# Kernel optimization log

Hardware: AMD Instinct MI355X
Metric: run time of the kernel (lower is better)

## Reference

```python
import jax, jax.numpy as jnp
import numpy as np

SHIFT, REDUCE = 3, 2
B, L, E, H = 64, 512, 300, 256


def _make_transitions():
    # Left-branching valid parse: S S R S R S R ... (L shifts, L-1 reduces)
    T = 2 * L - 1
    tr = np.full(T, REDUCE, dtype=np.int64)
    tr[0] = SHIFT
    tr[1::2] = SHIFT
    return jnp.asarray(np.tile(tr[None, :], (B, 1)))


def setup_inputs() -> dict:
    key = jax.random.key(0)
    ks = jax.random.split(key, 5)
    s = 0.05
    return {
        "sentence": jax.random.normal(ks[0], (B, L, E), jnp.float32),
        "transitions": _make_transitions(),
        "W_word": jax.random.normal(ks[1], (E, 2 * H), jnp.float32) * s,
        "b_word": jnp.zeros((2 * H,), jnp.float32),
        "W_left": jax.random.normal(ks[2], (H, 5 * H), jnp.float32) * s,
        "W_right": jax.random.normal(ks[3], (H, 5 * H), jnp.float32) * s,
        "b_reduce": jnp.zeros((5 * H,), jnp.float32),
    }


def reference(sentence, transitions, W_word, b_word, W_left, W_right, b_reduce):
    Bsz, Ls, _ = sentence.shape
    Hs = W_left.shape[0]
    proj = sentence @ W_word + b_word                  # [B, L, 2H] (word projection; BN/dropout disabled)
    h_buf, c_buf = jnp.split(proj, 2, axis=2)          # buffers, each [B, L, H]
    T = transitions.shape[1]
    bidx = jnp.arange(Bsz)

    def step(carry, trans_t):
        sh, sc, ptr, bp = carry                        # thin stacks [B,T+2,H], pointers [B]
        shift = trans_t == SHIFT
        i1 = jnp.maximum(ptr - 1, 0)                   # right child (stack top)
        i2 = jnp.maximum(ptr - 2, 0)                   # left child
        hl, cl = sh[bidx, i2], sc[bidx, i2]
        hr, cr = sh[bidx, i1], sc[bidx, i1]
        g = hl @ W_left + hr @ W_right + b_reduce      # [B, 5H] TreeLSTM gates
        ig, flg, frg, og, ug = jnp.split(g, 5, axis=1)
        c_red = (jax.nn.sigmoid(flg) * cl + jax.nn.sigmoid(frg) * cr
                 + jax.nn.sigmoid(ig) * jnp.tanh(ug))
        h_red = jax.nn.sigmoid(og) * jnp.tanh(c_red)
        bsafe = jnp.minimum(bp, Ls - 1)
        val_h = jnp.where(shift[:, None], h_buf[bidx, bsafe], h_red)
        val_c = jnp.where(shift[:, None], c_buf[bidx, bsafe], c_red)
        pos = jnp.where(shift, ptr, i2)                # shift pushes at ptr; reduce writes at ptr-2
        sh = sh.at[bidx, pos].set(val_h)
        sc = sc.at[bidx, pos].set(val_c)
        ptr = ptr + jnp.where(shift, 1, -1)
        bp = bp + shift.astype(bp.dtype)
        return (sh, sc, ptr, bp), None

    sh0 = jnp.zeros((Bsz, T + 2, Hs), sentence.dtype)
    sc0 = jnp.zeros((Bsz, T + 2, Hs), sentence.dtype)
    ptr0 = jnp.zeros((Bsz,), jnp.int32)
    bp0 = jnp.zeros((Bsz,), jnp.int32)
    (sh, sc, ptr, _), _ = jax.lax.scan(
        step, (sh0, sc0, ptr0, bp0), jnp.swapaxes(transitions, 0, 1))
    return sh[bidx, jnp.maximum(ptr - 1, 0)]           # final stack top h: [B, H]
```

## Files before the change

### kernel.cpp

```cpp
#include <hip/hip_runtime.h>
#include <hip/hip_bf16.h>
#include <math.h>

#define BSZ   64
#define LSEQ  512
#define EDIM  300
#define HDIM  256
#define TLEN  1023
#define PROJW 512
#define GW    1280

#define NROW  8
#define NHID  8
#define RGBLK 32
#define NRG   8
#define NBLK  256
#define SLOTS 2

#define PROJ_N   (BSZ*LSEQ*PROJW)
#define STACKF   PROJ_N
#define STACK_N  (2*BSZ*SLOTS*2*HDIM)
#define FLAG_OFF (STACKF + STACK_N)
#define FLAGS_N  1024
#define ARR_OFF  (FLAG_OFF + FLAGS_N)
#define ARR_STRIDE 16

#define NODEBIT 0x80000000u
#define SENT    0xFFFFFFFFu
#define LROW    264
#define WPITCH  641

__global__ void __launch_bounds__(256)
proj_gemm(const float* __restrict__ A, const float* __restrict__ W,
          const float* __restrict__ bias, float* __restrict__ out) {
    __shared__ float As[8][65];
    __shared__ float Bs[8][64];
    const int tid = threadIdx.x;
    const int tx = tid & 15, ty = tid >> 4;
    const int bm = blockIdx.y, bn = blockIdx.x;

    float acc[4][4] = {};
    const int e  = tid * 2;
    const int ar = e >> 3, ac = e & 7;
    const int br = e >> 6, bc = e & 63;

    for (int k0 = 0; k0 < EDIM; k0 += 8) {
        __syncthreads();
        {
            const float* Ap = A + (size_t)(bm * 64 + ar) * EDIM;
            int gk = k0 + ac;
            As[ac][ar]     = (gk     < EDIM) ? Ap[gk]     : 0.f;
            As[ac + 1][ar] = (gk + 1 < EDIM) ? Ap[gk + 1] : 0.f;
            int gkb = k0 + br;
            float w0 = 0.f, w1 = 0.f;
            if (gkb < EDIM) {
                const float* Wp = W + (size_t)gkb * PROJW + bn * 64;
                w0 = Wp[bc]; w1 = Wp[bc + 1];
            }
            Bs[br][bc] = w0; Bs[br][bc + 1] = w1;
        }
        __syncthreads();
        #pragma unroll
        for (int kk = 0; kk < 8; ++kk) {
            float a[4], b[4];
            #pragma unroll
            for (int i = 0; i < 4; ++i) a[i] = As[kk][ty * 4 + i];
            #pragma unroll
            for (int j = 0; j < 4; ++j) b[j] = Bs[kk][tx * 4 + j];
            #pragma unroll
            for (int i = 0; i < 4; ++i)
                #pragma unroll
                for (int j = 0; j < 4; ++j)
                    acc[i][j] += a[i] * b[j];
        }
    }
    #pragma unroll
    for (int i = 0; i < 4; ++i) {
        const int row  = bm * 64 + ty * 4 + i;
        const int col0 = bn * 64 + tx * 4;
        float* op = out + (size_t)row * PROJW + col0;
        #pragma unroll
        for (int j = 0; j < 4; ++j) op[j] = acc[i][j] + bias[col0 + j];
    }
}

__global__ void flags_kernel(const int* __restrict__ trans, int* __restrict__ flags) {
    const int t = blockIdx.x * 256 + threadIdx.x;
    if (t >= TLEN) return;
    int f = 0;
    for (int b = 0; b < BSZ; ++b) f |= (trans[(size_t)b * TLEN + t] != 3) ? 1 : 0;
    flags[t] = f;
}

__device__ __forceinline__ unsigned encodeH(short tag, int slot, int grow) {
    if (tag >= 0)  return (unsigned)(((size_t)grow * LSEQ + (int)tag) * PROJW);
    if (tag <= -3) return SENT;
    const int par = (tag == -2) ? 1 : 0;
    return NODEBIT | (unsigned)(STACKF + ((par * BSZ + grow) * SLOTS + slot) * (2 * HDIM));
}

__device__ __forceinline__ float cohLoad(const float* ws, unsigned off) {
    return __uint_as_float(__hip_atomic_load((const unsigned*)ws + off,
                          __ATOMIC_RELAXED, __HIP_MEMORY_SCOPE_AGENT));
}
__device__ __forceinline__ float2 cohLoad2(const float* ws, unsigned off) {
    unsigned long long v = __hip_atomic_load((const unsigned long long*)(ws + off),
                          __ATOMIC_RELAXED, __HIP_MEMORY_SCOPE_AGENT);
    union { unsigned long long u; float2 f; } cv; cv.u = v;
    return cv.f;
}
__device__ __forceinline__ void cohStore(float* ws, unsigned off, float v) {
    __hip_atomic_store((unsigned*)ws + off, __float_as_uint(v),
                       __ATOMIC_RELAXED, __HIP_MEMORY_SCOPE_AGENT);
}

__device__ __forceinline__ float loadC(const float* ws, unsigned oh, int gn) {
    if (oh == SENT) return 0.f;
    if (oh & NODEBIT) return cohLoad(ws, (oh & ~NODEBIT) + HDIM + gn);
    return ws[oh + HDIM + gn];
}

__device__ __forceinline__ void stage_rows(float* __restrict__ buf,
    const unsigned* __restrict__ desc, const int* __restrict__ isred,
    const float* __restrict__ ws, int srow, int sc, bool nodePhase) {
    if (!isred[srow]) return;
    const unsigned oh = desc[srow];
    const int m = srow & 7;
    if (!nodePhase) {
        if (oh == SENT) {
            const float4 z = make_float4(0.f, 0.f, 0.f, 0.f);
            #pragma unroll
            for (int j = 0; j < 2; ++j) {
                const int Q = sc + 32 * j;
                *(float4*)&buf[srow * LROW + 4 * (Q ^ m)] = z;
            }
        } else if (!(oh & NODEBIT)) {
            const float4* s = (const float4*)(ws + oh);
            #pragma unroll
            for (int j = 0; j < 2; ++j) {
                const int Q = sc + 32 * j;
                *(float4*)&buf[srow * LROW + 4 * (Q ^ m)] = s[Q];
            }
        }
    } else if (oh != SENT && (oh & NODEBIT)) {
        const unsigned base = oh & ~NODEBIT;
        #pragma unroll
        for (int j = 0; j < 2; ++j) {
            const int Q = sc + 32 * j;
            const float2 lo = cohLoad2(ws, base + 4 * Q);
            const float2 hi = cohLoad2(ws, base + 4 * Q + 2);
            *(float4*)&buf[srow * LROW + 4 * (Q ^ m)] = make_float4(lo.x, lo.y, hi.x, hi.y);
        }
    }
}

__global__ void __launch_bounds__(256, 1)
scan_coop(const int* __restrict__ trans,
          const float* __restrict__ Wl, const float* __restrict__ Wr,
          const float* __restrict__ bred,
          float* __restrict__ ws, float* __restrict__ out) {
    __shared__ float4 wpack[NHID * WPITCH];
    __shared__ __align__(16) float hls[NROW * LROW];
    __shared__ __align__(16) float hrs[NROW * LROW];
    __shared__ __align__(16) float red[8 * NROW * NHID * 5];
    __shared__ unsigned tbits[NROW][32];
    __shared__ unsigned fbits[32];
    __shared__ short    tg[NROW][SLOTS];
    __shared__ unsigned d_hl[NROW], d_hr[NROW], d_wr[NROW], d_oh[NROW];
    __shared__ int      isred[NROW];

    const int tid   = threadIdx.x;
    const int cs    = blockIdx.x & 31;
    const int rg    = blockIdx.x >> 5;
    const int rbase = rg * NROW;
    const int n0    = cs * NHID;

    const int srow = tid >> 5, sc = tid & 31;
    const int colq = tid & 7;
    const int t4   = (tid >> 3) & 3;
    const int w8   = tid >> 5;

    const int* flags  = (const int*)(ws + FLAG_OFF);
    unsigned*  arr    = (unsigned*)(ws + ARR_OFF);
    unsigned*  myslot = &arr[(size_t)blockIdx.x * ARR_STRIDE];

    for (int idx = tid; idx < NHID * 640; idx += 256) {
        const int g = idx % 10, kq = (idx / 10) & 63, c = idx / 640;
        const int col  = n0 + c;
        const int gate = (g < 5) ? g : g - 5;
        const float* src = (g < 5) ? Wl : Wr;
        const int k0 = kq * 4;
        float4 v;
        v.x = src[(size_t)(k0 + 0) * GW + gate * HDIM + col];
        v.y = src[(size_t)(k0 + 1) * GW + gate * HDIM + col];
        v.z = src[(size_t)(k0 + 2) * GW + gate * HDIM + col];
        v.w = src[(size_t)(k0 + 3) * GW + gate * HDIM + col];
        wpack[c * WPITCH + kq * 10 + g] = v;
    }
    if (tid < NROW * 32) {
        const int r2 = tid >> 5, w = tid & 31;
        unsigned bits = 0;
        for (int j = 0; j < 32; ++j) {
            const int t = w * 32 + j;
            if (t < TLEN && trans[(size_t)(rbase + r2) * TLEN + t] == 3) bits |= (1u << j);
        }
        tbits[r2][w] = bits;
    }
    if (tid < 32) {
        unsigned bits = 0;
        for (int j = 0; j < 32; ++j) {
            const int t = tid * 32 + j;
            if (t < TLEN && flags[t]) bits |= (1u << j);
        }
        fbits[tid] = bits;
    }
    if (tid < NROW) {
        tg[tid][0] = -3; tg[tid][1] = -3;
        isred[tid] = 0;
    }

    float bv[5];
    #pragma unroll
    for (int g = 0; g < 5; ++g) bv[g] = bred[g * HDIM + n0 + colq];

    int ptr = 0, bp = 0;
    unsigned nbar = 0;
    __syncthreads();

    for (int t = 0; t < TLEN; ++t) {
        if (tid < NROW) {
            const int r = tid, grow = rbase + r;
            const int is_shift = (tbits[r][t >> 5] >> (t & 31)) & 1;
            if (is_shift) {
                int pos = ptr; if (pos < 0) pos = 0; if (pos > SLOTS - 1) pos = SLOTS - 1;
                tg[r][pos] = (short)min(bp, LSEQ - 1);
                ptr++; bp++;
                isred[r] = 0;
            } else {
                const int i1 = min(max(ptr - 1, 0), SLOTS - 1);
                const int i2 = min(max(ptr - 2, 0), SLOTS - 1);
                const short t1 = tg[r][i1], t2 = tg[r][i2];
                d_hl[r] = encodeH(t2, i2, grow);
                d_hr[r] = encodeH(t1, i1, grow);
                const int pnew = (t2 == -1) ? 1 : 0;
                d_wr[r] = (unsigned)(STACKF + ((pnew * BSZ + grow) * SLOTS + i2) * (2 * HDIM));
                tg[r][i2] = (short)(pnew ? -2 : -1);
                ptr--;
                isred[r] = 1;
            }
        }
        __syncthreads();

        if (!((fbits[t >> 5] >> (t & 31)) & 1)) continue;
        ++nbar;

        stage_rows(hls, d_hl, isred, ws, srow, sc, false);
        stage_rows(hrs, d_hr, isred, ws, srow, sc, false);

        if (tid < RGBLK) {
            const unsigned* slot = &arr[(size_t)(rg * RGBLK + tid) * ARR_STRIDE];
            while (__hip_atomic_load(slot, __ATOMIC_RELAXED, __HIP_MEMORY_SCOPE_AGENT) < nbar - 1)
                __builtin_amdgcn_s_sleep(1);
        }
        __syncthreads();

        stage_rows(hls, d_hl, isred, ws, srow, sc, true);
        stage_rows(hrs, d_hr, isred, ws, srow, sc, true);
        __syncthreads();

        float a[2][5];
        #pragma unroll
        for (int i = 0; i < 2; ++i)
            #pragma unroll
            for (int g = 0; g < 5; ++g) a[i][g] = 0.f;

        {
            const float4* wp = &wpack[colq * WPITCH + w8 * 80];
            #pragma unroll 2
            for (int j = 0; j < 8; ++j, wp += 10) {
                const int kq = w8 * 8 + j;
                float4 w[10];
                #pragma unroll
                for (int g = 0; g < 10; ++g) w[g] = wp[g];
                #pragma unroll
                for (int i = 0; i < 2; ++i) {
                    const int row = t4 * 2 + i;
                    const float4 x = *(const float4*)&hls[row * LROW + 4 * (kq ^ row)];
                    const float4 y = *(const float4*)&hrs[row * LROW + 4 * (kq ^ row)];
                    #pragma unroll
                    for (int g = 0; g < 5; ++g) {
                        a[i][g] += x.x * w[g].x + x.y * w[g].y + x.z * w[g].z + x.w * w[g].w;
                        a[i][g] += y.x * w[5+g].x + y.y * w[5+g].y + y.z * w[5+g].z + y.w * w[5+g].w;
                    }
                }
            }
        }

        #pragma unroll
        for (int i = 0; i < 2; ++i) {
            const int row = t4 * 2 + i;
            #pragma unroll
            for (int g = 0; g < 5; ++g)
                red[((w8 * 8 + row) * 8 + colq) * 5 + g] = a[i][g];
        }
        __syncthreads();

        if (tid < 64) {
            const int orow = tid >> 3;
            if (isred[orow]) {
                float s[5];
                #pragma unroll
                for (int g = 0; g < 5; ++g) s[g] = bv[g];
                #pragma unroll
                for (int w2 = 0; w2 < 8; ++w2)
                    #pragma unroll
                    for (int g = 0; g < 5; ++g)
                        s[g] += red[((w2 * 8 + orow) * 8 + colq) * 5 + g];
                const int gn = n0 + colq;
                const float cl = loadC(ws, d_hl[orow], gn);
                const float cr = loadC(ws, d_hr[orow], gn);
                const float si = 1.f / (1.f + expf(-s[0]));
                const float sl = 1.f / (1.f + expf(-s[1]));
                const float sr = 1.f / (1.f + expf(-s[2]));
                const float so = 1.f / (1.f + expf(-s[3]));
                const float c_red = sl * cl + sr * cr + si * tanhf(s[4]);
                const float h_red = so * tanhf(c_red);
                cohStore(ws, d_wr[orow] + gn, h_red);
                cohStore(ws, d_wr[orow] + HDIM + gn, c_red);
            }
        }

        asm volatile("s_waitcnt vmcnt(0)" ::: "memory");
        __syncthreads();
        if (tid == 0)
            __hip_atomic_store(myslot, nbar, __ATOMIC_RELAXED, __HIP_MEMORY_SCOPE_AGENT);
    }

    if (tid < RGBLK) {
        const unsigned* slot = &arr[(size_t)(rg * RGBLK + tid) * ARR_STRIDE];
        while (__hip_atomic_load(slot, __ATOMIC_RELAXED, __HIP_MEMORY_SCOPE_AGENT) < nbar)
            __builtin_amdgcn_s_sleep(1);
    }
    __syncthreads();
    if (tid < NROW) {
        const int top = min(max(ptr - 1, 0), SLOTS - 1);
        d_oh[tid] = encodeH(tg[tid][top], top, rbase + tid);
    }
    __syncthreads();
    if (tid < 64) {
        const int orow = tid >> 3;
        const int gn = n0 + colq;
        const unsigned oh = d_oh[orow];
        float v;
        if (oh == SENT) v = 0.f;
        else if (oh & NODEBIT) v = cohLoad(ws, (oh & ~NODEBIT) + gn);
        else v = ws[oh + gn];
        out[(size_t)(rbase + orow) * HDIM + gn] = v;
    }
}

extern "C" void kernel_launch(void* const* d_in, const int* in_sizes, int n_in,
                              void* d_out, int out_size, void* d_ws, size_t ws_size,
                              hipStream_t stream) {
    const float* sentence    = (const float*)d_in[0];
    const int*   transitions = (const int*)  d_in[1];
    const float* W_word      = (const float*)d_in[2];
    const float* b_word      = (const float*)d_in[3];
    const float* W_left      = (const float*)d_in[4];
    const float* W_right     = (const float*)d_in[5];
    const float* b_reduce    = (const float*)d_in[6];
    float* out  = (float*)d_out;
    float* ws_f = (float*)d_ws;

    hipMemsetAsync((char*)d_ws + (size_t)ARR_OFF * 4, 0,
                   (size_t)NBLK * ARR_STRIDE * 4, stream);

    flags_kernel<<<(TLEN + 255) / 256, 256, 0, stream>>>(
        transitions, (int*)(ws_f + FLAG_OFF));

    dim3 g1(PROJW / 64, (BSZ * LSEQ) / 64);
    proj_gemm<<<g1, 256, 0, stream>>>(sentence, W_word, b_word, ws_f);

    scan_coop<<<NBLK, 256, 0, stream>>>(transitions, W_left, W_right, b_reduce,
                                        ws_f, out);
}
```

Measured before the change: 3.105 ms.

## Keep TreeLSTM reduce weights in registers and split left/right children across threads

Each thread now preloads its slice of W_left or W_right into registers (40 float4) instead of reading packed weights from LDS every step. Threads are split by left/right child and by half of the rows, with a new XOR swizzle and a 16-way partial-sum reduction through LDS. Cell-state loads are hoisted ahead of the matvec, and the trailing block barrier before publishing the step flag is removed because only the first wave writes results. The costs are high register pressure with possible spilling, and a larger cross-thread reduction.

```diff
diff --git a/kernel.cpp b/kernel.cpp
--- a/kernel.cpp
+++ b/kernel.cpp
@@ -28,7 +28,9 @@
 #define NODEBIT 0x80000000u
 #define SENT    0xFFFFFFFFu
 #define LROW    264
-#define WPITCH  641
+#define HRO     (NROW*LROW + 4)
+#define RPITCH  328
+#define RROW    41
 
 __global__ void __launch_bounds__(256)
 proj_gemm(const float* __restrict__ A, const float* __restrict__ W,
@@ -120,26 +122,29 @@
     return ws[oh + HDIM + gn];
 }
 
+__device__ __forceinline__ int qswz(int Q, int row) {
+    return Q ^ row ^ ((Q >> 3) & 7);
+}
+
 __device__ __forceinline__ void stage_rows(float* __restrict__ buf,
     const unsigned* __restrict__ desc, const int* __restrict__ isred,
     const float* __restrict__ ws, int srow, int sc, bool nodePhase) {
     if (!isred[srow]) return;
     const unsigned oh = desc[srow];
-    const int m = srow & 7;
     if (!nodePhase) {
         if (oh == SENT) {
             const float4 z = make_float4(0.f, 0.f, 0.f, 0.f);
             #pragma unroll
             for (int j = 0; j < 2; ++j) {
                 const int Q = sc + 32 * j;
-                *(float4*)&buf[srow * LROW + 4 * (Q ^ m)] = z;
+                *(float4*)&buf[srow * LROW + 4 * qswz(Q, srow)] = z;
             }
         } else if (!(oh & NODEBIT)) {
             const float4* s = (const float4*)(ws + oh);
             #pragma unroll
             for (int j = 0; j < 2; ++j) {
                 const int Q = sc + 32 * j;
-                *(float4*)&buf[srow * LROW + 4 * (Q ^ m)] = s[Q];
+                *(float4*)&buf[srow * LROW + 4 * qswz(Q, srow)] = s[Q];
             }
         }
     } else if (oh != SENT && (oh & NODEBIT)) {
@@ -149,7 +154,7 @@
             const int Q = sc + 32 * j;
             const float2 lo = cohLoad2(ws, base + 4 * Q);
             const float2 hi = cohLoad2(ws, base + 4 * Q + 2);
-            *(float4*)&buf[srow * LROW + 4 * (Q ^ m)] = make_float4(lo.x, lo.y, hi.x, hi.y);
+            *(float4*)&buf[srow * LROW + 4 * qswz(Q, srow)] = make_float4(lo.x, lo.y, hi.x, hi.y);
         }
     }
 }
@@ -159,10 +164,8 @@
           const float* __restrict__ Wl, const float* __restrict__ Wr,
           const float* __restrict__ bred,
           float* __restrict__ ws, float* __restrict__ out) {
-    __shared__ float4 wpack[NHID * WPITCH];
-    __shared__ __align__(16) float hls[NROW * LROW];
-    __shared__ __align__(16) float hrs[NROW * LROW];
-    __shared__ __align__(16) float red[8 * NROW * NHID * 5];
+    __shared__ __align__(16) float hbuf[HRO + NROW * LROW];
+    __shared__ __align__(16) float red[16 * RPITCH];
     __shared__ unsigned tbits[NROW][32];
     __shared__ unsigned fbits[32];
     __shared__ short    tg[NROW][SLOTS];
@@ -177,34 +180,39 @@
 
     const int srow = tid >> 5, sc = tid & 31;
     const int colq = tid & 7;
-    const int t4   = (tid >> 3) & 3;
+    const int rh   = (tid >> 3) & 1;
+    const int m    = (tid >> 4) & 1;
     const int w8   = tid >> 5;
+    const int gn   = n0 + colq;
 
     const int* flags  = (const int*)(ws + FLAG_OFF);
     unsigned*  arr    = (unsigned*)(ws + ARR_OFF);
     unsigned*  myslot = &arr[(size_t)blockIdx.x * ARR_STRIDE];
 
-    for (int idx = tid; idx < NHID * 640; idx += 256) {
-        const int g = idx % 10, kq = (idx / 10) & 63, c = idx / 640;
-        const int col  = n0 + c;
-        const int gate = (g < 5) ? g : g - 5;
-        const float* src = (g < 5) ? Wl : Wr;
-        const int k0 = kq * 4;
-        float4 v;
-        v.x = src[(size_t)(k0 + 0) * GW + gate * HDIM + col];
-        v.y = src[(size_t)(k0 + 1) * GW + gate * HDIM + col];
-        v.z = src[(size_t)(k0 + 2) * GW + gate * HDIM + col];
-        v.w = src[(size_t)(k0 + 3) * GW + gate * HDIM + col];
-        wpack[c * WPITCH + kq * 10 + g] = v;
+    float4 w[8][5];
+    {
+        const float* src = (m == 0) ? Wl : Wr;
+        const int kbase = w8 * 32;
+        #pragma unroll
+        for (int j = 0; j < 8; ++j) {
+            const int k0 = kbase + j * 4;
+            #pragma unroll
+            for (int g = 0; g < 5; ++g) {
+                w[j][g].x = src[(size_t)(k0 + 0) * GW + g * HDIM + gn];
+                w[j][g].y = src[(size_t)(k0 + 1) * GW + g * HDIM + gn];
+                w[j][g].z = src[(size_t)(k0 + 2) * GW + g * HDIM + gn];
+                w[j][g].w = src[(size_t)(k0 + 3) * GW + g * HDIM + gn];
+            }
+        }
     }
     if (tid < NROW * 32) {
-        const int r2 = tid >> 5, w = tid & 31;
+        const int r2 = tid >> 5, wd = tid & 31;
         unsigned bits = 0;
         for (int j = 0; j < 32; ++j) {
-            const int t = w * 32 + j;
+            const int t = wd * 32 + j;
             if (t < TLEN && trans[(size_t)(rbase + r2) * TLEN + t] == 3) bits |= (1u << j);
         }
-        tbits[r2][w] = bits;
+        tbits[r2][wd] = bits;
     }
     if (tid < 32) {
         unsigned bits = 0;
@@ -221,7 +229,7 @@
 
     float bv[5];
     #pragma unroll
-    for (int g = 0; g < 5; ++g) bv[g] = bred[g * HDIM + n0 + colq];
+    for (int g = 0; g < 5; ++g) bv[g] = bred[g * HDIM + gn];
 
     int ptr = 0, bp = 0;
     unsigned nbar = 0;
@@ -254,8 +262,8 @@
         if (!((fbits[t >> 5] >> (t & 31)) & 1)) continue;
         ++nbar;
 
-        stage_rows(hls, d_hl, isred, ws, srow, sc, false);
-        stage_rows(hrs, d_hr, isred, ws, srow, sc, false);
+        stage_rows(hbuf,       d_hl, isred, ws, srow, sc, false);
+        stage_rows(hbuf + HRO, d_hr, isred, ws, srow, sc, false);
 
         if (tid < RGBLK) {
             const unsigned* slot = &arr[(size_t)(rg * RGBLK + tid) * ARR_STRIDE];
@@ -264,44 +272,51 @@
         }
         __syncthreads();
 
-        stage_rows(hls, d_hl, isred, ws, srow, sc, true);
-        stage_rows(hrs, d_hr, isred, ws, srow, sc, true);
-        __syncthreads();
-
-        float a[2][5];
-        #pragma unroll
-        for (int i = 0; i < 2; ++i)
-            #pragma unroll
-            for (int g = 0; g < 5; ++g) a[i][g] = 0.f;
+        stage_rows(hbuf,       d_hl, isred, ws, srow, sc, true);
+        stage_rows(hbuf + HRO, d_hr, isred, ws, srow, sc, true);
+        __syncthreads();
+
+        float cl = 0.f, cr = 0.f;
+        if (tid < 64) {
+            const int orow = tid >> 3;
+            if (isred[orow]) {
+                cl = loadC(ws, d_hl[orow], gn);
+                cr = loadC(ws, d_hr[orow], gn);
+            }
+        }
+
+        float acc[4][5];
+        #pragma unroll
+        for (int r = 0; r < 4; ++r)
+            #pragma unroll
+            for (int g = 0; g < 5; ++g) acc[r][g] = 0.f;
 
         {
-            const float4* wp = &wpack[colq * WPITCH + w8 * 80];
-            #pragma unroll 2
-            for (int j = 0; j < 8; ++j, wp += 10) {
+            const float* hb = hbuf + m * HRO;
+            #pragma unroll
+            for (int j = 0; j < 8; ++j) {
                 const int kq = w8 * 8 + j;
-                float4 w[10];
-                #pragma unroll
-                for (int g = 0; g < 10; ++g) w[g] = wp[g];
-                #pragma unroll
-                for (int i = 0; i < 2; ++i) {
-                    const int row = t4 * 2 + i;
-                    const float4 x = *(const float4*)&hls[row * LROW + 4 * (kq ^ row)];
-                    const float4 y = *(const float4*)&hrs[row * LROW + 4 * (kq ^ row)];
+                #pragma unroll
+                for (int r = 0; r < 4; ++r) {
+                    const int row = rh * 4 + r;
+                    const float4 x = *(const float4*)&hb[row * LROW + 4 * qswz(kq, row)];
                     #pragma unroll
-                    for (int g = 0; g < 5; ++g) {
-                        a[i][g] += x.x * w[g].x + x.y * w[g].y + x.z * w[g].z + x.w * w[g].w;
-                        a[i][g] += y.x * w[5+g].x + y.y * w[5+g].y + y.z * w[5+g].z + y.w * w[5+g].w;
-                    }
+                    for (int g = 0; g < 5; ++g)
+                        acc[r][g] += x.x * w[j][g].x + x.y * w[j][g].y
+                                   + x.z * w[j][g].z + x.w * w[j][g].w;
                 }
             }
         }
 
-        #pragma unroll
-        for (int i = 0; i < 2; ++i) {
-            const int row = t4 * 2 + i;
-            #pragma unroll
-            for (int g = 0; g < 5; ++g)
-                red[((w8 * 8 + row) * 8 + colq) * 5 + g] = a[i][g];
+        {
+            const int g16 = w8 * 2 + m;
+            #pragma unroll
+            for (int r = 0; r < 4; ++r) {
+                const int row = rh * 4 + r;
+                #pragma unroll
+                for (int g = 0; g < 5; ++g)
+                    red[g16 * RPITCH + row * RROW + colq * 5 + g] = acc[r][g];
+            }
         }
         __syncthreads();
 
@@ -312,13 +327,10 @@
                 #pragma unroll
                 for (int g = 0; g < 5; ++g) s[g] = bv[g];
                 #pragma unroll
-                for (int w2 = 0; w2 < 8; ++w2)
+                for (int q = 0; q < 16; ++q)
                     #pragma unroll
                     for (int g = 0; g < 5; ++g)
-                        s[g] += red[((w2 * 8 + orow) * 8 + colq) * 5 + g];
-                const int gn = n0 + colq;
-                const float cl = loadC(ws, d_hl[orow], gn);
-                const float cr = loadC(ws, d_hr[orow], gn);
+                        s[g] += red[q * RPITCH + orow * RROW + colq * 5 + g];
                 const float si = 1.f / (1.f + expf(-s[0]));
                 const float sl = 1.f / (1.f + expf(-s[1]));
                 const float sr = 1.f / (1.f + expf(-s[2]));
@@ -328,12 +340,10 @@
                 cohStore(ws, d_wr[orow] + gn, h_red);
                 cohStore(ws, d_wr[orow] + HDIM + gn, c_red);
             }
-        }
-
-        asm volatile("s_waitcnt vmcnt(0)" ::: "memory");
-        __syncthreads();
-        if (tid == 0)
-            __hip_atomic_store(myslot, nbar, __ATOMIC_RELAXED, __HIP_MEMORY_SCOPE_AGENT);
+            asm volatile("s_waitcnt vmcnt(0)" ::: "memory");
+            if (tid == 0)
+                __hip_atomic_store(myslot, nbar, __ATOMIC_RELAXED, __HIP_MEMORY_SCOPE_AGENT);
+        }
     }
 
     if (tid < RGBLK) {
@@ -349,7 +359,6 @@
     __syncthreads();
     if (tid < 64) {
         const int orow = tid >> 3;
-        const int gn = n0 + colq;
         const unsigned oh = d_oh[orow];
         float v;
         if (oh == SENT) v = 0.f;
```

Result: faster. 2.813 ms (-9.4%).
